# Optimization experiments

Measured on AMD Instinct MI355X. Metric: run time of the kernel, lower is better.

The kernel has to match this reference:

```python
import jax, jax.numpy as jnp
import numpy as np

NUM_CHANNELS = 64
IN_FEATURES = 256
OUT_FEATURES = 256
B = 128
N = 2048


def setup_inputs() -> dict:
    key = jax.random.key(0)
    k_x, k_c, k_w, k_b = jax.random.split(key, 4)
    x = jax.random.normal(k_x, (B, N, IN_FEATURES), dtype=jnp.float32)
    channels = jax.random.randint(k_c, (N,), 0, NUM_CHANNELS, dtype=jnp.int64)
    # kaiming_uniform_(a=sqrt(5)) over fan_in -> bound = 1/sqrt(fan_in)
    wb = 1.0 / np.sqrt(IN_FEATURES)
    weight = jax.random.uniform(k_w, (NUM_CHANNELS, OUT_FEATURES, IN_FEATURES),
                                dtype=jnp.float32, minval=-wb, maxval=wb)
    bias = jax.random.uniform(k_b, (NUM_CHANNELS, OUT_FEATURES),
                              dtype=jnp.float32, minval=-wb, maxval=wb)
    return {"x": x, "channels": channels, "weight": weight, "bias": bias}


def reference(x, channels, weight, bias):
    # Gather per-point weights/biases by channel id (shared across batch).
    w = weight[channels]          # [N, out, in]
    b = bias[channels]            # [N, out]
    # Equivalent to bmm over the point axis: [B,N,in] x [N,out,in] -> [B,N,out]
    y = jnp.einsum('bni,noi->bno', x, w)
    y = y + b                     # broadcast over batch
    y = jnp.tanh(y)               # activation=True
    y = y + x                     # residual mode 1 (out == in)
    return (y, channels)
```

## Files before the change

kernel.cpp:

```cpp
#include <hip/hip_runtime.h>
#include <hip/hip_bf16.h>


#define B_SZ  128
#define N_SZ  2048

typedef __attribute__((ext_vector_type(8))) __bf16 bf16x8;
typedef __attribute__((ext_vector_type(4))) float  f32x4;

__device__ __forceinline__ unsigned f2bf1(float f) {
    union { float f; unsigned u; } v; v.f = f;
    return (v.u + 0x7fffu + ((v.u >> 16) & 1u)) >> 16;
}
__device__ __forceinline__ int pack2(float lo, float hi) {
    return (int)(f2bf1(lo) | (f2bf1(hi) << 16));
}
__device__ __forceinline__ float bf2f(unsigned u16) {
    union { unsigned u; float f; } v; v.u = u16 << 16;
    return v.f;
}
__device__ __forceinline__ float tanh_fast(float s) {
    float a = fabsf(s);
    float t = __expf(-2.0f * a);
    float r = (1.0f - t) * __builtin_amdgcn_rcpf(1.0f + t);
    return s < 0.0f ? -r : r;
}

__global__ __launch_bounds__(512, 4) void channel_dense_kernel(
    const float* __restrict__ x, const int* __restrict__ channels,
    const float* __restrict__ weight, const float* __restrict__ bias,
    float* __restrict__ y)
{
    __shared__ __align__(16) unsigned char smem[65536 + 16384];
    unsigned char* sA = smem;
    unsigned char* sB = smem + 65536;

    const int n   = blockIdx.x;
    const int tid = threadIdx.x;
    const int c   = channels[n];
    const float* wch = weight + (size_t)c * 65536;

    const int bo = tid >> 1;
    const int bh = tid & 1;
    const float* wbase = wch + bo * 256 + bh * 16;
    float4 w0, w1, w2, w3;
    #define WLOAD(kt) do { const float* p_ = wbase + (kt) * 32;             \
        w0 = *(const float4*)(p_);     w1 = *(const float4*)(p_ + 4);       \
        w2 = *(const float4*)(p_ + 8); w3 = *(const float4*)(p_ + 12); } while (0)

    const int sb_lin   = bo * 64 + bh * 32;
    const int sb_swz   = (bo & 7) << 4;
    const int sb_byte0 = (sb_lin)      ^ sb_swz;
    const int sb_byte1 = (sb_lin + 16) ^ sb_swz;
    #define SB_WRITE() do {                                                 \
        int4 q0, q1;                                                        \
        q0.x = pack2(w0.x, w0.y); q0.y = pack2(w0.z, w0.w);                 \
        q0.z = pack2(w1.x, w1.y); q0.w = pack2(w1.z, w1.w);                 \
        q1.x = pack2(w2.x, w2.y); q1.y = pack2(w2.z, w2.w);                 \
        q1.z = pack2(w3.x, w3.y); q1.w = pack2(w3.z, w3.w);                 \
        *(int4*)(sB + sb_byte0) = q0;                                       \
        *(int4*)(sB + sb_byte1) = q1; } while (0)

    WLOAD(0);

    {
        const int row = tid >> 2;
        const int sub = tid & 3;
        const float* xrow = x + ((size_t)row * N_SZ + n) * 256 + sub * 64;
        const int swz = (row & 7) << 4;
        #pragma unroll
        for (int j = 0; j < 8; ++j) {
            float4 f0 = *(const float4*)(xrow + j * 8);
            float4 f1 = *(const float4*)(xrow + j * 8 + 4);
            int4 p;
            p.x = pack2(f0.x, f0.y); p.y = pack2(f0.z, f0.w);
            p.z = pack2(f1.x, f1.y); p.w = pack2(f1.z, f1.w);
            int byte = (sub * 2 + (j >> 2)) * 8192 + ((row * 64 + (j & 3) * 16) ^ swz);
            *(int4*)(sA + byte) = p;
        }
    }

    SB_WRITE();
    WLOAD(1);
    __syncthreads();

    const int lane = tid & 63;
    const int wv   = tid >> 6;
    const int wo   = wv & 3;
    const int wb   = wv >> 2;
    const int lr   = lane & 15;
    const int lg4  = lane >> 4;
    const int lane_part = ((lr * 64 + lg4 * 16) ^ ((lr & 7) << 4));
    const int wf_base = lane_part + wo * 4096;
    const int xf_base = lane_part + wb * 4096;

    f32x4 acc[4][4] = {};

    #pragma unroll
    for (int kt = 0; kt < 8; ++kt) {
        bf16x8 wf[4], xf[4];
        #pragma unroll
        for (int mo = 0; mo < 4; ++mo)
            wf[mo] = *(const bf16x8*)(sB + wf_base + mo * 1024);
        #pragma unroll
        for (int nb = 0; nb < 4; ++nb)
            xf[nb] = *(const bf16x8*)(sA + xf_base + nb * 1024 + kt * 8192);
        #pragma unroll
        for (int mo = 0; mo < 4; ++mo)
            #pragma unroll
            for (int nb = 0; nb < 4; ++nb)
                acc[mo][nb] = __builtin_amdgcn_mfma_f32_16x16x32_bf16(wf[mo], xf[nb], acc[mo][nb], 0, 0, 0);

        if (kt < 7) {
            __syncthreads();
            SB_WRITE();
            if (kt < 6) WLOAD(kt + 2);
            __syncthreads();
        }
    }

    const float* bch = bias + (size_t)c * 256;
    #pragma unroll
    for (int mo = 0; mo < 4; ++mo) {
        const int o0 = wo * 64 + mo * 16 + lg4 * 4;
        const float4 bv = *(const float4*)(bch + o0);
        const int kt_r  = o0 >> 5;
        const int intra = (o0 & 31) * 2;
        #pragma unroll
        for (int nb = 0; nb < 4; ++nb) {
            const int b = wb * 64 + nb * 16 + lr;
            const int rbyte = kt_r * 8192 + ((b * 64 + intra) ^ ((b & 7) << 4));
            uint2 rv = *(const uint2*)(sA + rbyte);
            float4 out;
            out.x = tanh_fast(acc[mo][nb][0] + bv.x) + bf2f(rv.x & 0xffffu);
            out.y = tanh_fast(acc[mo][nb][1] + bv.y) + bf2f(rv.x >> 16);
            out.z = tanh_fast(acc[mo][nb][2] + bv.z) + bf2f(rv.y & 0xffffu);
            out.w = tanh_fast(acc[mo][nb][3] + bv.w) + bf2f(rv.y >> 16);
            *(float4*)(y + ((size_t)b * N_SZ + n) * 256 + o0) = out;
        }
    }
    #undef WLOAD
    #undef SB_WRITE
}

__global__ void channels_copy_kernel(const int* __restrict__ ch, float* __restrict__ out) {
    int i = blockIdx.x * 256 + threadIdx.x;
    if (i < N_SZ) out[i] = (float)ch[i];
}

extern "C" void kernel_launch(void* const* d_in, const int* in_sizes, int n_in,
                              void* d_out, int out_size, void* d_ws, size_t ws_size,
                              hipStream_t stream) {
    const float* x        = (const float*)d_in[0];
    const int*   channels = (const int*)d_in[1];
    const float* weight   = (const float*)d_in[2];
    const float* bias     = (const float*)d_in[3];
    float* y = (float*)d_out;

    channel_dense_kernel<<<dim3(N_SZ), dim3(512), 0, stream>>>(x, channels, weight, bias, y);
    channels_copy_kernel<<<dim3(N_SZ / 256), dim3(256), 0, stream>>>(
        channels, y + (size_t)B_SZ * N_SZ * 256);
}
```

Measured before the change: 219.4 us.

## Pre-convert weights to bf16 workspace, sort points by channel, async-stage weight tiles

Adds a pre-pass that converts all channel weights once to a swizzled bf16 layout in workspace, and a counting sort that orders points by channel. The main kernel is split into two blocks per point (half the batch each), remapped so blocks sharing a channel run together for L2 reuse. Weight tiles are streamed with direct global-to-LDS loads into a double buffer, which removes the per-block fp32 conversion and cuts one of the two barriers per k-step. The cost is two extra launches, the whole weight tensor re-converted on every call, and each weight tile now read by twice as many blocks.

```diff
diff --git a/kernel.cpp b/kernel.cpp
--- a/kernel.cpp
+++ b/kernel.cpp
@@ -2,8 +2,7 @@
 #include <hip/hip_bf16.h>
 
 
-#define B_SZ  128
-#define N_SZ  2048
+#define N_SZ 2048
 
 typedef __attribute__((ext_vector_type(8))) __bf16 bf16x8;
 typedef __attribute__((ext_vector_type(4))) float  f32x4;
@@ -25,111 +24,131 @@
     float r = (1.0f - t) * __builtin_amdgcn_rcpf(1.0f + t);
     return s < 0.0f ? -r : r;
 }
+__device__ __forceinline__ void gl_lds16(const void* g, void* l) {
+    __builtin_amdgcn_global_load_lds(
+        (const __attribute__((address_space(1))) unsigned int*)g,
+        (__attribute__((address_space(3))) unsigned int*)l, 16, 0, 0);
+}
 
-__global__ __launch_bounds__(512, 4) void channel_dense_kernel(
+__global__ __launch_bounds__(1024) void sort_kernel(const int* __restrict__ channels,
+                                                    int* __restrict__ perm) {
+    __shared__ int cnt[64], off[64];
+    const int t = threadIdx.x;
+    if (t < 64) cnt[t] = 0;
+    __syncthreads();
+    const int n0 = t, n1 = t + 1024;
+    const int c0 = channels[n0], c1 = channels[n1];
+    atomicAdd(&cnt[c0], 1);
+    atomicAdd(&cnt[c1], 1);
+    __syncthreads();
+    if (t == 0) { int s = 0; for (int i = 0; i < 64; ++i) { off[i] = s; s += cnt[i]; } }
+    __syncthreads();
+    int p0 = atomicAdd(&off[c0], 1); perm[p0] = n0;
+    int p1 = atomicAdd(&off[c1], 1); perm[p1] = n1;
+}
+
+__global__ __launch_bounds__(256) void wconv_kernel(const float* __restrict__ w,
+                                                    unsigned char* __restrict__ wsW) {
+    const int t   = blockIdx.x * 256 + threadIdx.x;
+    const int c   = t >> 13;
+    const int rem = t & 8191;
+    const int o   = rem >> 5;
+    const int ch  = rem & 31;
+    const int kt  = ch >> 2;
+    const int j   = ch & 3;
+    const float* src = w + ((((size_t)c << 8) | o) << 8) + (ch << 3);
+    float4 f0 = *(const float4*)(src);
+    float4 f1 = *(const float4*)(src + 4);
+    int4 p;
+    p.x = pack2(f0.x, f0.y); p.y = pack2(f0.z, f0.w);
+    p.z = pack2(f1.x, f1.y); p.w = pack2(f1.z, f1.w);
+    const int dst = (c << 17) + (kt << 14) + ((o * 64 + j * 16) ^ ((o & 7) << 4));
+    *(int4*)(wsW + dst) = p;
+}
+
+__global__ __launch_bounds__(256, 2) void channel_dense_kernel(
     const float* __restrict__ x, const int* __restrict__ channels,
-    const float* __restrict__ weight, const float* __restrict__ bias,
-    float* __restrict__ y)
+    const int* __restrict__ perm, const unsigned char* __restrict__ wsW,
+    const float* __restrict__ bias, float* __restrict__ y)
 {
-    __shared__ __align__(16) unsigned char smem[65536 + 16384];
-    unsigned char* sA = smem;
-    unsigned char* sB = smem + 65536;
+    __shared__ __align__(16) unsigned char sA[32768];
+    __shared__ __align__(16) unsigned char sB[2][16384];
 
-    const int n   = blockIdx.x;
-    const int tid = threadIdx.x;
-    const int c   = channels[n];
-    const float* wch = weight + (size_t)c * 65536;
+    const int g    = blockIdx.x;
+    const int lg   = (g & 7) * 512 + (g >> 3);
+    const int n    = perm[lg >> 1];
+    const int half = lg & 1;
+    const int tid  = threadIdx.x;
+    const int c    = channels[n];
+    const unsigned char* wc = wsW + ((size_t)c << 17);
 
-    const int bo = tid >> 1;
-    const int bh = tid & 1;
-    const float* wbase = wch + bo * 256 + bh * 16;
-    float4 w0, w1, w2, w3;
-    #define WLOAD(kt) do { const float* p_ = wbase + (kt) * 32;             \
-        w0 = *(const float4*)(p_);     w1 = *(const float4*)(p_ + 4);       \
-        w2 = *(const float4*)(p_ + 8); w3 = *(const float4*)(p_ + 12); } while (0)
+    const int lane = tid & 63;
+    const int wv   = tid >> 6;
 
-    const int sb_lin   = bo * 64 + bh * 32;
-    const int sb_swz   = (bo & 7) << 4;
-    const int sb_byte0 = (sb_lin)      ^ sb_swz;
-    const int sb_byte1 = (sb_lin + 16) ^ sb_swz;
-    #define SB_WRITE() do {                                                 \
-        int4 q0, q1;                                                        \
-        q0.x = pack2(w0.x, w0.y); q0.y = pack2(w0.z, w0.w);                 \
-        q0.z = pack2(w1.x, w1.y); q0.w = pack2(w1.z, w1.w);                 \
-        q1.x = pack2(w2.x, w2.y); q1.y = pack2(w2.z, w2.w);                 \
-        q1.z = pack2(w3.x, w3.y); q1.w = pack2(w3.z, w3.w);                 \
-        *(int4*)(sB + sb_byte0) = q0;                                       \
-        *(int4*)(sB + sb_byte1) = q1; } while (0)
+    #define STAGE_W(kt, buf) do {                                              \
+        const unsigned char* s_ = wc + ((kt) << 14) + (wv << 12) + (lane << 4);\
+        unsigned char* d_ = sB[buf] + (wv << 12);                              \
+        gl_lds16(s_,        d_);                                               \
+        gl_lds16(s_ + 1024, d_ + 1024);                                        \
+        gl_lds16(s_ + 2048, d_ + 2048);                                        \
+        gl_lds16(s_ + 3072, d_ + 3072); } while (0)
 
-    WLOAD(0);
+    STAGE_W(0, 0);
 
     {
-        const int row = tid >> 2;
+        const int r   = tid >> 2;
         const int sub = tid & 3;
-        const float* xrow = x + ((size_t)row * N_SZ + n) * 256 + sub * 64;
-        const int swz = (row & 7) << 4;
+        const float* xr = x + ((size_t)(half * 64 + r) * N_SZ + n) * 256 + sub * 64;
+        const int swz = (r & 7) << 4;
         #pragma unroll
         for (int j = 0; j < 8; ++j) {
-            float4 f0 = *(const float4*)(xrow + j * 8);
-            float4 f1 = *(const float4*)(xrow + j * 8 + 4);
+            float4 f0 = *(const float4*)(xr + j * 8);
+            float4 f1 = *(const float4*)(xr + j * 8 + 4);
             int4 p;
             p.x = pack2(f0.x, f0.y); p.y = pack2(f0.z, f0.w);
             p.z = pack2(f1.x, f1.y); p.w = pack2(f1.z, f1.w);
-            int byte = (sub * 2 + (j >> 2)) * 8192 + ((row * 64 + (j & 3) * 16) ^ swz);
+            const int byte = (sub * 2 + (j >> 2)) * 4096 + ((r * 64 + (j & 3) * 16) ^ swz);
             *(int4*)(sA + byte) = p;
         }
     }
-
-    SB_WRITE();
-    WLOAD(1);
     __syncthreads();
 
-    const int lane = tid & 63;
-    const int wv   = tid >> 6;
-    const int wo   = wv & 3;
-    const int wb   = wv >> 2;
     const int lr   = lane & 15;
     const int lg4  = lane >> 4;
-    const int lane_part = ((lr * 64 + lg4 * 16) ^ ((lr & 7) << 4));
-    const int wf_base = lane_part + wo * 4096;
-    const int xf_base = lane_part + wb * 4096;
+    const int lanebyte = (lr * 64 + lg4 * 16) ^ ((lr & 7) << 4);
 
     f32x4 acc[4][4] = {};
 
     #pragma unroll
     for (int kt = 0; kt < 8; ++kt) {
+        if (kt < 7) STAGE_W(kt + 1, (kt + 1) & 1);
         bf16x8 wf[4], xf[4];
         #pragma unroll
         for (int mo = 0; mo < 4; ++mo)
-            wf[mo] = *(const bf16x8*)(sB + wf_base + mo * 1024);
+            wf[mo] = *(const bf16x8*)(sB[kt & 1] + (wv << 12) + (mo << 10) + lanebyte);
         #pragma unroll
         for (int nb = 0; nb < 4; ++nb)
-            xf[nb] = *(const bf16x8*)(sA + xf_base + nb * 1024 + kt * 8192);
+            xf[nb] = *(const bf16x8*)(sA + (kt << 12) + (nb << 10) + lanebyte);
         #pragma unroll
         for (int mo = 0; mo < 4; ++mo)
             #pragma unroll
             for (int nb = 0; nb < 4; ++nb)
                 acc[mo][nb] = __builtin_amdgcn_mfma_f32_16x16x32_bf16(wf[mo], xf[nb], acc[mo][nb], 0, 0, 0);
-
-        if (kt < 7) {
-            __syncthreads();
-            SB_WRITE();
-            if (kt < 6) WLOAD(kt + 2);
-            __syncthreads();
-        }
+        __syncthreads();
     }
 
     const float* bch = bias + (size_t)c * 256;
     #pragma unroll
     for (int mo = 0; mo < 4; ++mo) {
-        const int o0 = wo * 64 + mo * 16 + lg4 * 4;
+        const int o0 = wv * 64 + mo * 16 + lg4 * 4;
         const float4 bv = *(const float4*)(bch + o0);
         const int kt_r  = o0 >> 5;
         const int intra = (o0 & 31) * 2;
         #pragma unroll
         for (int nb = 0; nb < 4; ++nb) {
-            const int b = wb * 64 + nb * 16 + lr;
-            const int rbyte = kt_r * 8192 + ((b * 64 + intra) ^ ((b & 7) << 4));
+            const int rl = nb * 16 + lr;
+            const int b  = half * 64 + rl;
+            const int rbyte = (kt_r << 12) + ((rl * 64 + intra) ^ ((rl & 7) << 4));
             uint2 rv = *(const uint2*)(sA + rbyte);
             float4 out;
             out.x = tanh_fast(acc[mo][nb][0] + bv.x) + bf2f(rv.x & 0xffffu);
@@ -139,8 +158,7 @@
             *(float4*)(y + ((size_t)b * N_SZ + n) * 256 + o0) = out;
         }
     }
-    #undef WLOAD
-    #undef SB_WRITE
+    #undef STAGE_W
 }
 
 __global__ void channels_copy_kernel(const int* __restrict__ ch, float* __restrict__ out) {
@@ -157,7 +175,13 @@
     const float* bias     = (const float*)d_in[3];
     float* y = (float*)d_out;
 
-    channel_dense_kernel<<<dim3(N_SZ), dim3(512), 0, stream>>>(x, channels, weight, bias, y);
+    unsigned char* wsW = (unsigned char*)d_ws;
+    int* perm = (int*)(wsW + (64u << 17));
+
+    sort_kernel<<<dim3(1), dim3(1024), 0, stream>>>(channels, perm);
+    wconv_kernel<<<dim3(2048), dim3(256), 0, stream>>>(weight, wsW);
+    channel_dense_kernel<<<dim3(4096), dim3(256), 0, stream>>>(
+        x, channels, perm, wsW, bias, y);
     channels_copy_kernel<<<dim3(N_SZ / 256), dim3(256), 0, stream>>>(
-        channels, y + (size_t)B_SZ * N_SZ * 256);
+        channels, y + (size_t)128 * N_SZ * 256);
 }
```

New measurement: 181.5 us. 17.3% less time.
